# Kernel tuning notes

Hardware: AMD Instinct MI355X
Metric: run time of the kernel (lower is better)

The kernel has to match this reference:

```python
import jax, jax.numpy as jnp
import numpy as np

B, S, H, NH = 4, 4096, 1024, 16
HD = H // NH  # head_dim = 64


def setup_inputs() -> dict:
    key = jax.random.key(0)
    ks = jax.random.split(key, 8)
    scale = 0.02
    return {
        "hidden_states": jax.random.normal(ks[0], (B, S, H), dtype=jnp.float32),
        "attention_mask": jnp.ones((B, S), dtype=jnp.float32),
        "Wq": jax.random.normal(ks[1], (H, H), dtype=jnp.float32) * scale,
        "bq": jnp.zeros((H,), dtype=jnp.float32),
        "Wk": jax.random.normal(ks[2], (H, H), dtype=jnp.float32) * scale,
        "bk": jnp.zeros((H,), dtype=jnp.float32),
        "Wv": jax.random.normal(ks[3], (H, H), dtype=jnp.float32) * scale,
        "bv": jnp.zeros((H,), dtype=jnp.float32),
        "Wo": jax.random.normal(ks[4], (H, H), dtype=jnp.float32) * scale,
        "bo": jnp.zeros((H,), dtype=jnp.float32),
    }


def _heads(x):
    # [B,S,H] -> [B,NH,S,HD]
    b, s, _ = x.shape
    return x.reshape(b, s, NH, HD).transpose(0, 2, 1, 3)


def reference(hidden_states, attention_mask, Wq, bq, Wk, bk, Wv, bv, Wo, bo):
    b, s, _ = hidden_states.shape
    q = _heads(hidden_states @ Wq.T + bq)
    k = _heads(hidden_states @ Wk.T + bk)
    v = _heads(hidden_states @ Wv.T + bv)

    m = attention_mask[:, None, :, None]  # [B,1,S,1]
    k = k * m
    v = v * m

    # Faithful to the torch code: kv_i = matmul(k_i[b,h,1,d], v_i[b,h,d,1])
    # is the SCALAR dot product k_t . v_t, broadcast-added to the [d,d] state.
    # => state_t = (cumsum_t k_t.v_t) * ones(d,d)
    # => o_t = state_t @ q_t = (cumsum_t k_t.v_t) * sum_j q_t[j], same for every i.
    dots = jnp.einsum('bhsd,bhsd->bhs', k, v)        # scalar k.v per step
    cum = jnp.cumsum(dots, axis=-1)                  # running state scalar
    qsum = jnp.sum(q, axis=-1)                       # [B,NH,S]
    o = jnp.broadcast_to((cum * qsum)[..., None], q.shape)  # [B,NH,S,HD]

    out = o.transpose(0, 2, 1, 3).reshape(b, s, NH * HD)
    out = out @ Wo.T + bo  # dropout is identity (eval / p handled as 0)

    # final state: last cumulative scalar broadcast over the [d,d] matrix
    state = jnp.broadcast_to(cum[:, :, -1, None, None], (b, NH, HD, HD))
    return out, state
```

## Files before the change

kernel.cpp:

```cpp
#include <hip/hip_runtime.h>
#include <hip/hip_bf16.h>


typedef __attribute__((ext_vector_type(4))) float f32x4;
typedef __attribute__((ext_vector_type(8))) short bf16x8;
typedef __attribute__((ext_vector_type(8))) unsigned short u16x8;
typedef unsigned int u32;

#define GLDS16(g, l)                                                            \
  __builtin_amdgcn_global_load_lds((const __attribute__((address_space(1))) u32*)(g), \
                                   (__attribute__((address_space(3))) u32*)(l), 16, 0, 0)
#define MFMA16(a, b, c) __builtin_amdgcn_mfma_f32_16x16x32_bf16(a, b, c, 0, 0, 0)
#define LGK0 do { asm volatile("s_waitcnt lgkmcnt(0)" ::: "memory"); \
                  __builtin_amdgcn_sched_barrier(0); } while (0)

__device__ __forceinline__ unsigned short f2bf(float f) {
  union { float f; u32 u; } x; x.f = f;
  u32 r = (x.u + 0x7fffu + ((x.u >> 16) & 1u)) >> 16;
  return (unsigned short)r;
}

__device__ __forceinline__ bf16x8 pack8(const f32x4& lo, const f32x4& hi) {
  union { bf16x8 v; u32 w[4]; } r;
  union { __hip_bfloat162 h; u32 u; } c;
  c.h = __float22bfloat162_rn(make_float2(lo.x, lo.y)); r.w[0] = c.u;
  c.h = __float22bfloat162_rn(make_float2(lo.z, lo.w)); r.w[1] = c.u;
  c.h = __float22bfloat162_rn(make_float2(hi.x, hi.y)); r.w[2] = c.u;
  c.h = __float22bfloat162_rn(make_float2(hi.z, hi.w)); r.w[3] = c.u;
  return r.v;
}

__global__ void k_prep(const float* __restrict__ Wq, const float* __restrict__ bq,
                       const float* __restrict__ Wk, const float* __restrict__ bk,
                       const float* __restrict__ Wv, const float* __restrict__ bv,
                       const float* __restrict__ Wo,
                       unsigned short* __restrict__ Wkb, unsigned short* __restrict__ Wvb,
                       unsigned short* __restrict__ SWb, float* __restrict__ WosT,
                       float* __restrict__ scal) {
  int blk = blockIdx.x, t = threadIdx.x;
  if (blk < 2048) {
    const float* src = (blk < 1024) ? Wk : Wv;
    unsigned short* dst = (blk < 1024) ? Wkb : Wvb;
    size_t i = ((size_t)(blk & 1023) * 256 + t) * 4;
    f32x4 v = *(const f32x4*)(src + i);
    dst[i + 0] = f2bf(v.x); dst[i + 1] = f2bf(v.y);
    dst[i + 2] = f2bf(v.z); dst[i + 3] = f2bf(v.w);
  } else {
    int b2 = blk - 2048;
    if (b2 < 128) {
      int o = b2 * 256 + t;
      int r = o >> 10, c = o & 1023;
      float s = 0.f;
      if (r < 16) {
        for (int d = 0; d < 64; ++d) s += Wq[(size_t)(r * 64 + d) * 1024 + c];
      } else {
        int h = r - 16;
        for (int d = 0; d < 64; ++d) {
          int j = h * 64 + d;
          s += bv[j] * Wk[(size_t)j * 1024 + c] + bk[j] * Wv[(size_t)j * 1024 + c];
        }
      }
      SWb[o] = f2bf(s);
    } else if (b2 < 192) {
      int o = (b2 - 128) * 256 + t;
      int h = o >> 10, j = o & 1023;
      float s = 0.f;
      for (int d = 0; d < 64; ++d) s += Wo[(size_t)j * 1024 + h * 64 + d];
      WosT[o] = s;
    } else {
      if (t < 16) {
        float s = 0.f;
        for (int d = 0; d < 64; ++d) s += bq[t * 64 + d];
        scal[t] = s;
      } else if (t < 32) {
        int h = t - 16;
        float s = 0.f;
        for (int d = 0; d < 64; ++d) s += bk[h * 64 + d] * bv[h * 64 + d];
        scal[t] = s;
      }
    }
  }
}

#define NT 32
__global__ __launch_bounds__(512, 2) void k_dualgemm(
    const float* __restrict__ X,
    const unsigned short* __restrict__ Wkb,
    const unsigned short* __restrict__ Wvb,
    const unsigned short* __restrict__ SWb,
    float* __restrict__ dotsT, float* __restrict__ qsumT, float* __restrict__ dotbT) {
  extern __shared__ __align__(16) char ldsb[];
  float* Af = (float*)ldsb;
  unsigned short* Bb = (unsigned short*)(ldsb + 98304);
  unsigned short* Sw = (unsigned short*)(ldsb + 147456);
  int orig = blockIdx.x;
  int wg = (orig & 7) * 64 + (orig >> 3);
  int bx = wg & 7, by = wg >> 3;
  int row0 = by << 8, col0 = bx << 7;
  int tid = threadIdx.x, wid = tid >> 6, lane = tid & 63;
  int wrM = wid >> 1, wcN = wid & 1;
  int fr = lane & 15, fg = lane >> 4;
  bool side = (bx == 0);
  bool stageSW = side && (wid < 2);

  const float* sA[4];
#pragma unroll
  for (int c = 0; c < 4; ++c) {
    int U = c * 512 + tid, r = U >> 3, g = (U & 7) ^ (r & 7);
    sA[c] = X + (size_t)(row0 + r) * 1024 + g * 4;
  }
  const unsigned short *sK, *sV, *sS;
  {
    int r = tid >> 2, s = tid & 3, g = s ^ ((r >> 1) & 3);
    sK = Wkb + (size_t)(col0 + r) * 1024 + g * 8;
    sV = Wvb + (size_t)(col0 + r) * 1024 + g * 8;
    int rs = (tid & 127) >> 2, ss = tid & 3, gs = ss ^ ((rs >> 1) & 3);
    sS = SWb + (size_t)rs * 1024 + gs * 8;
  }
  int dA = tid << 2;
  int dB = tid << 3;
  int dS = tid << 3;

  int keyA = fr & 7, s0 = (2 * fg) ^ keyA;
  int aoffL[4], aoffH[4];
#pragma unroll
  for (int mi = 0; mi < 4; ++mi) {
    int R = wrM * 64 + mi * 16 + fr;
    aoffL[mi] = R * 32 + s0 * 4;
    aoffH[mi] = R * 32 + (s0 ^ 1) * 4;
  }
  int ubo = (fg ^ ((fr >> 1) & 3)) << 3;
  int bko[4], bvo[4];
#pragma unroll
  for (int ni = 0; ni < 4; ++ni) {
    bko[ni] = (wcN * 64 + ni * 16 + fr) * 32 + ubo;
    bvo[ni] = 4096 + (wcN * 64 + ni * 16 + fr) * 32 + ubo;
  }
  int swo = (wcN * 16 + fr) * 32 + ubo;

  f32x4 ck[4][4] = {{0}}, cv[4][4] = {{0}};
  f32x4 qa[4] = {0, 0, 0, 0};

#pragma unroll
  for (int p = 0; p < 2; ++p) {
    int ko = p << 5;
#pragma unroll
    for (int c = 0; c < 4; ++c) GLDS16(sA[c] + ko, Af + p * 8192 + c * 2048 + dA);
    GLDS16(sK + ko, Bb + p * 8192 + dB);
    GLDS16(sV + ko, Bb + p * 8192 + 4096 + dB);
    if (stageSW) GLDS16(sS + ko, Sw + p * 1024 + dS);
  }
  asm volatile("s_waitcnt vmcnt(6)" ::: "memory");
  __builtin_amdgcn_s_barrier();

  int bufR = 0;
  for (int t = 0; t < NT; ++t) {
    const float* ArB = Af + bufR * 8192;
    const unsigned short* BkB = Bb + bufR * 8192;
    const unsigned short* SwB = Sw + bufR * 1024;
    const int bufW = (bufR + 2 >= 3) ? bufR - 1 : bufR + 2;
    const int ko = (t + 2) << 5;
    const bool st = (t + 2 < NT);

    f32x4 alo[4], ahi[4];
#pragma unroll
    for (int mi = 0; mi < 4; ++mi) {
      alo[mi] = *(const f32x4*)(ArB + aoffL[mi]);
      ahi[mi] = *(const f32x4*)(ArB + aoffH[mi]);
    }
    if (st) {
#pragma unroll
      for (int c = 0; c < 4; ++c) GLDS16(sA[c] + ko, Af + bufW * 8192 + c * 2048 + dA);
    }
    bf16x8 bk[4];
#pragma unroll
    for (int ni = 0; ni < 4; ++ni) bk[ni] = *(const bf16x8*)(BkB + bko[ni]);
    LGK0;
    bf16x8 a[4];
#pragma unroll
    for (int mi = 0; mi < 4; ++mi) a[mi] = pack8(alo[mi], ahi[mi]);
    __builtin_amdgcn_s_setprio(1);
#pragma unroll
    for (int mi = 0; mi < 4; ++mi)
#pragma unroll
      for (int ni = 0; ni < 4; ++ni)
        ck[mi][ni] = MFMA16(a[mi], bk[ni], ck[mi][ni]);
    __builtin_amdgcn_s_setprio(0);

    bf16x8 bv[4], sw;
#pragma unroll
    for (int ni = 0; ni < 4; ++ni) bv[ni] = *(const bf16x8*)(BkB + bvo[ni]);
    if (side) sw = *(const bf16x8*)(SwB + swo);
    if (st) {
      GLDS16(sK + ko, Bb + bufW * 8192 + dB);
      GLDS16(sV + ko, Bb + bufW * 8192 + 4096 + dB);
      if (stageSW) GLDS16(sS + ko, Sw + bufW * 1024 + dS);
    }
    LGK0;
    __builtin_amdgcn_s_setprio(1);
#pragma unroll
    for (int mi = 0; mi < 4; ++mi)
#pragma unroll
      for (int ni = 0; ni < 4; ++ni)
        cv[mi][ni] = MFMA16(a[mi], bv[ni], cv[mi][ni]);
    if (side) {
#pragma unroll
      for (int mi = 0; mi < 4; ++mi) qa[mi] = MFMA16(a[mi], sw, qa[mi]);
    }
    __builtin_amdgcn_s_setprio(0);

    if (t <= NT - 3) { asm volatile("s_waitcnt vmcnt(6)" ::: "memory"); }
    else             { asm volatile("s_waitcnt vmcnt(0)" ::: "memory"); }
    __builtin_amdgcn_s_barrier();
    bufR = (bufR + 1 >= 3) ? 0 : bufR + 1;
  }

  float part[4][4];
#pragma unroll
  for (int mi = 0; mi < 4; ++mi)
#pragma unroll
    for (int q = 0; q < 4; ++q) {
      float s = 0.f;
#pragma unroll
      for (int ni = 0; ni < 4; ++ni) s += ck[mi][ni][q] * cv[mi][ni][q];
      part[mi][q] = s;
    }
#pragma unroll
  for (int r = 0; r < 4; ++r) {
#pragma unroll
    for (int mi = 0; mi < 4; ++mi)
#pragma unroll
      for (int q = 0; q < 4; ++q)
        part[mi][q] += __shfl_xor(part[mi][q], 1 << r, 64);
  }
  int h = bx * 2 + wcN;
  if (fr == 0) {
#pragma unroll
    for (int mi = 0; mi < 4; ++mi)
#pragma unroll
      for (int q = 0; q < 4; ++q)
        dotsT[(size_t)h * 16384 + row0 + wrM * 64 + mi * 16 + fg * 4 + q] = part[mi][q];
  }
  if (side) {
    float* dst = (wcN == 0) ? qsumT : dotbT;
#pragma unroll
    for (int mi = 0; mi < 4; ++mi)
#pragma unroll
      for (int q = 0; q < 4; ++q)
        dst[(size_t)fr * 16384 + row0 + wrM * 64 + mi * 16 + fg * 4 + q] = qa[mi][q];
  }
}

__global__ void k_cumsum(const float* __restrict__ dotsT, const float* __restrict__ dotbT,
                         const float* __restrict__ qsumT, const float* __restrict__ scal,
                         const float* __restrict__ mask,
                         float* __restrict__ coef, float* __restrict__ state) {
  __shared__ float csum[256];
  int b = blockIdx.x >> 4, h = blockIdx.x & 15;
  int t = threadIdx.x;
  float bqs = scal[h], dbc = scal[16 + h];
  size_t m0 = (size_t)b * 4096;
  const float* dro = dotsT + (size_t)h * 16384 + m0;
  const float* dbo = dotbT + (size_t)h * 16384 + m0;
  const float* qso = qsumT + (size_t)h * 16384 + m0;
  const float* mko = mask + m0;
  float loc[16], run = 0.f;
  int s0 = t * 16;
#pragma unroll
  for (int i = 0; i < 16; ++i) {
    int ii = s0 + i;
    float mk = mko[ii];
    float d = (dro[ii] + dbo[ii] + dbc) * mk * mk;
    run += d;
    loc[i] = run;
  }
  csum[t] = run;
  __syncthreads();
  for (int off = 1; off < 256; off <<= 1) {
    float v = (t >= off) ? csum[t - off] : 0.f;
    __syncthreads();
    csum[t] += v;
    __syncthreads();
  }
  float prefix = csum[t] - run;
#pragma unroll
  for (int i = 0; i < 16; ++i) {
    int ii = s0 + i;
    float cum = prefix + loc[i];
    coef[(m0 + ii) * 16 + h] = cum * (qso[ii] + bqs);
  }
  float total = csum[255];
  float* sp = state + (size_t)(b * 16 + h) * 4096;
  for (int i = t; i < 4096; i += 256) sp[i] = total;
}

__global__ __launch_bounds__(256) void k_outgemm(const float* __restrict__ coef,
                                                 const float* __restrict__ WosT,
                                                 const float* __restrict__ bo,
                                                 float* __restrict__ out) {
  int t = threadIdx.x;
  int j0 = t * 4;
  f32x4 w4[16];
#pragma unroll
  for (int hh = 0; hh < 16; ++hh) w4[hh] = *(const f32x4*)&WosT[hh * 1024 + j0];
  f32x4 bov = *(const f32x4*)&bo[j0];
  size_t m0 = (size_t)blockIdx.x * 32;
  for (int mi = 0; mi < 32; ++mi) {
    size_t m = m0 + mi;
    const float* cm = &coef[m * 16];
    f32x4 acc = bov;
#pragma unroll
    for (int hh = 0; hh < 16; ++hh) acc += w4[hh] * cm[hh];
    *(f32x4*)&out[m * 1024 + j0] = acc;
  }
}

extern "C" void kernel_launch(void* const* d_in, const int* in_sizes, int n_in,
                              void* d_out, int out_size, void* d_ws, size_t ws_size,
                              hipStream_t stream) {
  const float* X    = (const float*)d_in[0];
  const float* mask = (const float*)d_in[1];
  const float* Wq   = (const float*)d_in[2];
  const float* bq   = (const float*)d_in[3];
  const float* Wk   = (const float*)d_in[4];
  const float* bk   = (const float*)d_in[5];
  const float* Wv   = (const float*)d_in[6];
  const float* bv   = (const float*)d_in[7];
  const float* Wo   = (const float*)d_in[8];
  const float* bo   = (const float*)d_in[9];
  float* out   = (float*)d_out;
  float* state = out + (size_t)16384 * 1024;

  char* w = (char*)d_ws;
  unsigned short* Wkb = (unsigned short*)w; w += (size_t)1024 * 1024 * 2;
  unsigned short* Wvb = (unsigned short*)w; w += (size_t)1024 * 1024 * 2;
  unsigned short* SWb = (unsigned short*)w; w += (size_t)32 * 1024 * 2;
  float* WosT  = (float*)w; w += (size_t)16 * 1024 * 4;
  float* scal  = (float*)w; w += 256;
  float* dotsT = (float*)w; w += (size_t)16 * 16384 * 4;
  float* qsumT = (float*)w; w += (size_t)16 * 16384 * 4;
  float* dotbT = (float*)w; w += (size_t)16 * 16384 * 4;
  float* coef  = (float*)w; w += (size_t)16384 * 16 * 4;

  (void)hipFuncSetAttribute((const void*)k_dualgemm,
                            hipFuncAttributeMaxDynamicSharedMemorySize, 153600);

  hipLaunchKernelGGL(k_prep,     dim3(2241), dim3(256), 0, stream,
                     Wq, bq, Wk, bk, Wv, bv, Wo, Wkb, Wvb, SWb, WosT, scal);
  hipLaunchKernelGGL(k_dualgemm, dim3(512),  dim3(512), 153600, stream, X, Wkb, Wvb, SWb,
                     dotsT, qsumT, dotbT);
  hipLaunchKernelGGL(k_cumsum,   dim3(64),   dim3(256), 0, stream, dotsT, dotbT, qsumT, scal,
                     mask, coef, state);
  hipLaunchKernelGGL(k_outgemm,  dim3(512),  dim3(256), 0, stream, coef, WosT, bo, out);
}
```

Before: 118.3 us.

## Convert X to bf16 via registers before LDS and use 4-stage buffering

The fp32 X tile is no longer copied into LDS and converted on every read. Each thread now loads it into registers one step ahead, packs it to bf16 and writes the bf16 result to LDS. This halves the LDS footprint and read traffic for A and removes the repeated per-warp pack work. The buffer ring grows to four stages, with K/V weights prefetched three steps ahead through global_load_lds. The trade-off is more register pressure and a synchronous global load plus LDS write inside the loop, which could expose latency.

```diff
diff --git a/kernel.cpp b/kernel.cpp
--- a/kernel.cpp
+++ b/kernel.cpp
@@ -83,16 +83,14 @@
 }
 
 #define NT 32
+#define BUFS 17408
 __global__ __launch_bounds__(512, 2) void k_dualgemm(
     const float* __restrict__ X,
     const unsigned short* __restrict__ Wkb,
     const unsigned short* __restrict__ Wvb,
     const unsigned short* __restrict__ SWb,
     float* __restrict__ dotsT, float* __restrict__ qsumT, float* __restrict__ dotbT) {
-  extern __shared__ __align__(16) char ldsb[];
-  float* Af = (float*)ldsb;
-  unsigned short* Bb = (unsigned short*)(ldsb + 98304);
-  unsigned short* Sw = (unsigned short*)(ldsb + 147456);
+  extern __shared__ __align__(16) unsigned short lds[];
   int orig = blockIdx.x;
   int wg = (orig & 7) * 64 + (orig >> 3);
   int bx = wg & 7, by = wg >> 3;
@@ -101,84 +99,67 @@
   int wrM = wid >> 1, wcN = wid & 1;
   int fr = lane & 15, fg = lane >> 4;
   bool side = (bx == 0);
-  bool stageSW = side && (wid < 2);
-
-  const float* sA[4];
-#pragma unroll
-  for (int c = 0; c < 4; ++c) {
-    int U = c * 512 + tid, r = U >> 3, g = (U & 7) ^ (r & 7);
-    sA[c] = X + (size_t)(row0 + r) * 1024 + g * 4;
-  }
-  const unsigned short *sK, *sV, *sS;
-  {
-    int r = tid >> 2, s = tid & 3, g = s ^ ((r >> 1) & 3);
-    sK = Wkb + (size_t)(col0 + r) * 1024 + g * 8;
-    sV = Wvb + (size_t)(col0 + r) * 1024 + g * 8;
-    int rs = (tid & 127) >> 2, ss = tid & 3, gs = ss ^ ((rs >> 1) & 3);
-    sS = SWb + (size_t)rs * 1024 + gs * 8;
-  }
-  int dA = tid << 2;
-  int dB = tid << 3;
-  int dS = tid << 3;
-
-  int keyA = fr & 7, s0 = (2 * fg) ^ keyA;
-  int aoffL[4], aoffH[4];
-#pragma unroll
-  for (int mi = 0; mi < 4; ++mi) {
-    int R = wrM * 64 + mi * 16 + fr;
-    aoffL[mi] = R * 32 + s0 * 4;
-    aoffH[mi] = R * 32 + (s0 ^ 1) * 4;
-  }
+  bool swv = side && (wid < 2);
+
+  int rA = tid >> 2, sA = tid & 3;
+  int gA = sA ^ ((tid >> 3) & 3);
+  const float* pA0 = X + (size_t)(row0 + rA) * 1024 + gA * 8;
+  const float* pA1 = pA0 + (size_t)128 * 1024;
+  int wo0 = rA * 32 + sA * 8;
+  int wo1 = wo0 + 4096;
+
+  int rB = tid >> 2;
+  int uswB = (((tid & 3) ^ ((tid >> 3) & 3)) << 3);
+  const unsigned short* sK = Wkb + (size_t)(col0 + rB) * 1024 + uswB;
+  const unsigned short* sV = Wvb + (size_t)(col0 + rB) * 1024 + uswB;
+  const unsigned short* sS = SWb + (size_t)(tid >> 2) * 1024 + uswB;
+  int dK = 8192 + (wid << 9), dV = 12288 + (wid << 9), dS = 16384 + (wid << 9);
+
   int ubo = (fg ^ ((fr >> 1) & 3)) << 3;
-  int bko[4], bvo[4];
-#pragma unroll
-  for (int ni = 0; ni < 4; ++ni) {
-    bko[ni] = (wcN * 64 + ni * 16 + fr) * 32 + ubo;
-    bvo[ni] = 4096 + (wcN * 64 + ni * 16 + fr) * 32 + ubo;
-  }
-  int swo = (wcN * 16 + fr) * 32 + ubo;
+  int aro = (wrM * 64 + fr) * 32 + ubo;
+  int bro = (wcN * 64 + fr) * 32 + ubo;
+  int swo = 16384 + (wcN * 16 + fr) * 32 + ubo;
 
   f32x4 ck[4][4] = {{0}}, cv[4][4] = {{0}};
   f32x4 qa[4] = {0, 0, 0, 0};
 
-#pragma unroll
-  for (int p = 0; p < 2; ++p) {
-    int ko = p << 5;
-#pragma unroll
-    for (int c = 0; c < 4; ++c) GLDS16(sA[c] + ko, Af + p * 8192 + c * 2048 + dA);
-    GLDS16(sK + ko, Bb + p * 8192 + dB);
-    GLDS16(sV + ko, Bb + p * 8192 + 4096 + dB);
-    if (stageSW) GLDS16(sS + ko, Sw + p * 1024 + dS);
-  }
-  asm volatile("s_waitcnt vmcnt(6)" ::: "memory");
-  __builtin_amdgcn_s_barrier();
-
-  int bufR = 0;
+  {
+    f32x4 xl0 = *(const f32x4*)(pA0);     f32x4 xh0 = *(const f32x4*)(pA0 + 4);
+    f32x4 xl1 = *(const f32x4*)(pA1);     f32x4 xh1 = *(const f32x4*)(pA1 + 4);
+#pragma unroll
+    for (int p = 0; p < 3; ++p) {
+      int ko = p << 5;
+      GLDS16(sK + ko, lds + p * BUFS + dK);
+      GLDS16(sV + ko, lds + p * BUFS + dV);
+      if (swv) GLDS16(sS + ko, lds + p * BUFS + dS);
+    }
+    if (swv) { asm volatile("s_waitcnt vmcnt(6)" ::: "memory"); }
+    else     { asm volatile("s_waitcnt vmcnt(4)" ::: "memory"); }
+    *(bf16x8*)(lds + wo0) = pack8(xl0, xh0);
+    *(bf16x8*)(lds + wo1) = pack8(xl1, xh1);
+    asm volatile("s_waitcnt lgkmcnt(0)" ::: "memory");
+    __builtin_amdgcn_s_barrier();
+  }
+
   for (int t = 0; t < NT; ++t) {
-    const float* ArB = Af + bufR * 8192;
-    const unsigned short* BkB = Bb + bufR * 8192;
-    const unsigned short* SwB = Sw + bufR * 1024;
-    const int bufW = (bufR + 2 >= 3) ? bufR - 1 : bufR + 2;
-    const int ko = (t + 2) << 5;
-    const bool st = (t + 2 < NT);
-
-    f32x4 alo[4], ahi[4];
-#pragma unroll
-    for (int mi = 0; mi < 4; ++mi) {
-      alo[mi] = *(const f32x4*)(ArB + aoffL[mi]);
-      ahi[mi] = *(const f32x4*)(ArB + aoffH[mi]);
-    }
-    if (st) {
-#pragma unroll
-      for (int c = 0; c < 4; ++c) GLDS16(sA[c] + ko, Af + bufW * 8192 + c * 2048 + dA);
-    }
-    bf16x8 bk[4];
-#pragma unroll
-    for (int ni = 0; ni < 4; ++ni) bk[ni] = *(const bf16x8*)(BkB + bko[ni]);
+    const int rb = (t & 3) * BUFS;
+    const bool st1 = (t + 1 < NT);
+    const bool st3 = (t + 3 < NT);
+    const int ko1 = (t + 1) << 5;
+    const int ko3 = (t + 3) << 5;
+    const int wb3 = ((t + 3) & 3) * BUFS;
+
+    bf16x8 a[4], bk[4];
+#pragma unroll
+    for (int mi = 0; mi < 4; ++mi) a[mi] = *(const bf16x8*)(lds + rb + aro + mi * 512);
+#pragma unroll
+    for (int ni = 0; ni < 4; ++ni) bk[ni] = *(const bf16x8*)(lds + rb + 8192 + bro + ni * 512);
+    f32x4 xl0, xh0, xl1, xh1;
+    if (st1) {
+      xl0 = *(const f32x4*)(pA0 + ko1); xh0 = *(const f32x4*)(pA0 + ko1 + 4);
+      xl1 = *(const f32x4*)(pA1 + ko1); xh1 = *(const f32x4*)(pA1 + ko1 + 4);
+    }
     LGK0;
-    bf16x8 a[4];
-#pragma unroll
-    for (int mi = 0; mi < 4; ++mi) a[mi] = pack8(alo[mi], ahi[mi]);
     __builtin_amdgcn_s_setprio(1);
 #pragma unroll
     for (int mi = 0; mi < 4; ++mi)
@@ -189,12 +170,12 @@
 
     bf16x8 bv[4], sw;
 #pragma unroll
-    for (int ni = 0; ni < 4; ++ni) bv[ni] = *(const bf16x8*)(BkB + bvo[ni]);
-    if (side) sw = *(const bf16x8*)(SwB + swo);
-    if (st) {
-      GLDS16(sK + ko, Bb + bufW * 8192 + dB);
-      GLDS16(sV + ko, Bb + bufW * 8192 + 4096 + dB);
-      if (stageSW) GLDS16(sS + ko, Sw + bufW * 1024 + dS);
+    for (int ni = 0; ni < 4; ++ni) bv[ni] = *(const bf16x8*)(lds + rb + 12288 + bro + ni * 512);
+    if (side) sw = *(const bf16x8*)(lds + rb + swo);
+    if (st3) {
+      GLDS16(sK + ko3, lds + wb3 + dK);
+      GLDS16(sV + ko3, lds + wb3 + dV);
+      if (swv) GLDS16(sS + ko3, lds + wb3 + dS);
     }
     LGK0;
     __builtin_amdgcn_s_setprio(1);
@@ -209,10 +190,21 @@
     }
     __builtin_amdgcn_s_setprio(0);
 
-    if (t <= NT - 3) { asm volatile("s_waitcnt vmcnt(6)" ::: "memory"); }
-    else             { asm volatile("s_waitcnt vmcnt(0)" ::: "memory"); }
+    if (st1) {
+      if (t < NT - 3) {
+        if (swv) { asm volatile("s_waitcnt vmcnt(3)" ::: "memory"); }
+        else     { asm volatile("s_waitcnt vmcnt(2)" ::: "memory"); }
+      } else {
+        asm volatile("s_waitcnt vmcnt(0)" ::: "memory");
+      }
+      unsigned short* Aw = lds + ((t + 1) & 3) * BUFS;
+      *(bf16x8*)(Aw + wo0) = pack8(xl0, xh0);
+      *(bf16x8*)(Aw + wo1) = pack8(xl1, xh1);
+      asm volatile("s_waitcnt lgkmcnt(0)" ::: "memory");
+    } else {
+      asm volatile("s_waitcnt vmcnt(0)" ::: "memory");
+    }
     __builtin_amdgcn_s_barrier();
-    bufR = (bufR + 1 >= 3) ? 0 : bufR + 1;
   }
 
   float part[4][4];
@@ -343,11 +335,11 @@
   float* coef  = (float*)w; w += (size_t)16384 * 16 * 4;
 
   (void)hipFuncSetAttribute((const void*)k_dualgemm,
-                            hipFuncAttributeMaxDynamicSharedMemorySize, 153600);
+                            hipFuncAttributeMaxDynamicSharedMemorySize, 139264);
 
   hipLaunchKernelGGL(k_prep,     dim3(2241), dim3(256), 0, stream,
                      Wq, bq, Wk, bk, Wv, bv, Wo, Wkb, Wvb, SWb, WosT, scal);
-  hipLaunchKernelGGL(k_dualgemm, dim3(512),  dim3(512), 153600, stream, X, Wkb, Wvb, SWb,
+  hipLaunchKernelGGL(k_dualgemm, dim3(512),  dim3(512), 139264, stream, X, Wkb, Wvb, SWb,
                      dotsT, qsumT, dotbT);
   hipLaunchKernelGGL(k_cumsum,   dim3(64),   dim3(256), 0, stream, dotsT, dotbT, qsumT, scal,
                      mask, coef, state);
```

New measurement: 110.3 us. 6.8% less time.
